# Performance work log

Measured on AMD Instinct MI355X. Metric: run time of the kernel, lower is better.

Reference implementation:

```python
import jax, jax.numpy as jnp
import numpy as np

A = 0.5  # mixing coefficient `a` from __init__
B, S, C = 16, 4096, 512


def setup_inputs() -> dict:
    key = jax.random.key(0)
    k1, k2 = jax.random.split(key)
    predicted = jax.random.normal(k1, (B, S, C), dtype=jnp.float32)
    target = jax.random.randint(k2, (B, S), 0, C, dtype=jnp.int64)
    return {"predicted": predicted, "target": target}


def reference(predicted, target):
    # predicted: [B, S, C] logits, target: [B, S] int class ids.
    b, s, c = predicted.shape
    am = jnp.argmax(predicted, axis=-1)              # [B, S] per-position top-1 class (topk(1)[1])
    lse = jax.nn.logsumexp(predicted, axis=-1)       # [B, S]

    # counts[i, j, v] = #positions s with target[i,s]==j and argmax==v
    bidx = jnp.arange(b)[:, None]
    counts = jnp.zeros((b, c, c), dtype=jnp.int32).at[bidx, target, am].add(1)
    n = counts.sum(axis=-1)                          # [B, C] occurrences of class j in target[i]
    # torch.mode returns the smallest of the most common values; argmax over class value
    # returns the first (smallest) index achieving the max count, matching that tie-break.
    m = jnp.argmax(counts, axis=-1)                  # [B, C] mode label per (i, j)

    # pred_m[i, j, s] = predicted[i, s, m[i, j]]
    pred_m = predicted[jnp.arange(b)[:, None, None],
                       jnp.arange(s)[None, None, :],
                       m[:, :, None]]                # [B, C, S]
    # per-position CE against constant label m: lse - logit[m]
    term = lse[:, None, :] - pred_m                  # [B, C, S]

    maskT = target[:, None, :] == jnp.arange(c)[None, :, None]  # [B, C, S]
    eq_sum = jnp.sum(jnp.where(maskT, term, 0.0), axis=-1)      # [B, C]
    ne_sum = term.sum(axis=-1) - eq_sum                          # [B, C]

    nf = n.astype(predicted.dtype)
    present = n > 0
    eq_loss = eq_sum / jnp.maximum(nf, 1.0)
    ne_mean = ne_sum / jnp.maximum(s - nf, 1.0)
    ne_loss = 1.0 / jnp.where(present & (ne_mean != 0), ne_mean, 1.0)
    val = eq_loss * (1.0 - A) + A * ne_loss          # [B, C]

    keep = present & (val != 0)                      # cipherLoss[cipherLoss != 0]
    total = jnp.where(keep, val, 0.0).sum()
    cnt = jnp.maximum(keep.sum(), 1).astype(predicted.dtype)
    return total / cnt
```

## Files before the change

kernel.cpp:

```cpp
#include <hip/hip_runtime.h>
#include <cstdint>
#include <cstddef>

#define PB 16
#define PS 4096
#define PC 512

__global__ __launch_bounds__(256) void k1_rows(const float* __restrict__ pred,
                                               int* __restrict__ am,
                                               float* __restrict__ lse,
                                               float* __restrict__ colsum) {
    const int t = threadIdx.x, w = t >> 6, l = t & 63;
    const int rowBase = blockIdx.x * 16 + w * 4;
    const int b = rowBase >> 12;
    const float* base = pred + (size_t)rowBase * PC + 4 * l;

    float4 va[4], vb[4];
    #pragma unroll
    for (int r = 0; r < 4; ++r) {
        va[r] = *(const float4*)(base + r * PC);
        vb[r] = *(const float4*)(base + r * PC + 256);
    }

    float mv[4]; int mi[4];
    #pragma unroll
    for (int r = 0; r < 4; ++r) {
        float m = va[r].x; int i0 = 4 * l;
        if (va[r].y > m) { m = va[r].y; i0 = 4 * l + 1; }
        if (va[r].z > m) { m = va[r].z; i0 = 4 * l + 2; }
        if (va[r].w > m) { m = va[r].w; i0 = 4 * l + 3; }
        if (vb[r].x > m) { m = vb[r].x; i0 = 256 + 4 * l; }
        if (vb[r].y > m) { m = vb[r].y; i0 = 256 + 4 * l + 1; }
        if (vb[r].z > m) { m = vb[r].z; i0 = 256 + 4 * l + 2; }
        if (vb[r].w > m) { m = vb[r].w; i0 = 256 + 4 * l + 3; }
        mv[r] = m; mi[r] = i0;
    }

    #pragma unroll
    for (int off = 1; off < 64; off <<= 1) {
        #pragma unroll
        for (int r = 0; r < 4; ++r) {
            float ov = __shfl_xor(mv[r], off, 64);
            int   oi = __shfl_xor(mi[r], off, 64);
            if (ov > mv[r] || (ov == mv[r] && oi < mi[r])) { mv[r] = ov; mi[r] = oi; }
        }
    }

    float ss[4];
    #pragma unroll
    for (int r = 0; r < 4; ++r) {
        ss[r] = __expf(va[r].x - mv[r]) + __expf(va[r].y - mv[r])
              + __expf(va[r].z - mv[r]) + __expf(va[r].w - mv[r])
              + __expf(vb[r].x - mv[r]) + __expf(vb[r].y - mv[r])
              + __expf(vb[r].z - mv[r]) + __expf(vb[r].w - mv[r]);
    }
    #pragma unroll
    for (int off = 1; off < 64; off <<= 1) {
        #pragma unroll
        for (int r = 0; r < 4; ++r) ss[r] += __shfl_xor(ss[r], off, 64);
    }

    float l0 = mv[0] + __logf(ss[0]);
    float l1 = mv[1] + __logf(ss[1]);
    float l2 = mv[2] + __logf(ss[2]);
    float l3 = mv[3] + __logf(ss[3]);

    if (l == 0) {
        *(float4*)(lse + rowBase) = make_float4(l0, l1, l2, l3);
        *(int4*)(am + rowBase) = make_int4(mi[0], mi[1], mi[2], mi[3]);
    }

    float cs0 = va[0].x + va[1].x + va[2].x + va[3].x;
    float cs1 = va[0].y + va[1].y + va[2].y + va[3].y;
    float cs2 = va[0].z + va[1].z + va[2].z + va[3].z;
    float cs3 = va[0].w + va[1].w + va[2].w + va[3].w;
    float cs4 = vb[0].x + vb[1].x + vb[2].x + vb[3].x;
    float cs5 = vb[0].y + vb[1].y + vb[2].y + vb[3].y;
    float cs6 = vb[0].z + vb[1].z + vb[2].z + vb[3].z;
    float cs7 = vb[0].w + vb[1].w + vb[2].w + vb[3].w;

    __shared__ float lds[4][PC];
    lds[w][4 * l + 0] = cs0; lds[w][4 * l + 1] = cs1;
    lds[w][4 * l + 2] = cs2; lds[w][4 * l + 3] = cs3;
    lds[w][256 + 4 * l + 0] = cs4; lds[w][256 + 4 * l + 1] = cs5;
    lds[w][256 + 4 * l + 2] = cs6; lds[w][256 + 4 * l + 3] = cs7;
    __syncthreads();
    for (int c = t; c < PC; c += 256) {
        float s = lds[0][c] + lds[1][c] + lds[2][c] + lds[3][c];
        atomicAdd(&colsum[(b << 9) + c], s);
    }
}

__global__ __launch_bounds__(1024) void k_tail(const float* __restrict__ pred,
                                               const int* __restrict__ target,
                                               const int* __restrict__ am,
                                               const float* __restrict__ lse,
                                               const float* __restrict__ colsum,
                                               float* __restrict__ acc,
                                               int* __restrict__ done,
                                               float* __restrict__ out) {
    __shared__ float ldsLse[PS];
    __shared__ int   sbucket[PS];
    __shared__ int   cnt[PC];
    __shared__ int   offsA[PC];
    __shared__ int   cur[PC];
    __shared__ float redL[16];
    __shared__ int   redS[8];
    __shared__ float redv[16], redk[16];

    const int b = blockIdx.x, t = threadIdx.x, w = t >> 6, l = t & 63;
    if (t < PC) cnt[t] = 0;
    __syncthreads();

    const int4*   tg4p = (const int4*)(target + (b << 12));
    const int4*   am4p = (const int4*)(am + (b << 12));
    const float4* ls4p = (const float4*)(lse + (b << 12));
    int4 tg4 = tg4p[t];
    int4 am4 = am4p[t];
    float4 ls4 = ls4p[t];
    ((float4*)ldsLse)[t] = ls4;
    atomicAdd(&cnt[tg4.x], 1);
    atomicAdd(&cnt[tg4.y], 1);
    atomicAdd(&cnt[tg4.z], 1);
    atomicAdd(&cnt[tg4.w], 1);
    float lacc = ls4.x + ls4.y + ls4.z + ls4.w;
    #pragma unroll
    for (int off = 1; off < 64; off <<= 1) lacc += __shfl_xor(lacc, off, 64);
    if (l == 0) redL[w] = lacc;
    __syncthreads();
    float Ls = 0.0f;
    #pragma unroll
    for (int j = 0; j < 16; ++j) Ls += redL[j];

    int x = 0, incl = 0;
    if (t < PC) {
        x = cnt[t];
        incl = x;
        #pragma unroll
        for (int off = 1; off < 64; off <<= 1) {
            int v = __shfl_up(incl, off, 64);
            if (l >= off) incl += v;
        }
        if (l == 63) redS[w] = incl;
    }
    __syncthreads();
    if (t < PC) {
        int woff = 0;
        #pragma unroll
        for (int j = 0; j < 8; ++j) woff += (j < w) ? redS[j] : 0;
        int excl = incl + woff - x;
        offsA[t] = excl;
        cur[t] = excl;
    }
    __syncthreads();

    {
        int pos;
        pos = atomicAdd(&cur[tg4.x], 1); sbucket[pos] = (4 * t + 0) | (am4.x << 12);
        pos = atomicAdd(&cur[tg4.y], 1); sbucket[pos] = (4 * t + 1) | (am4.y << 12);
        pos = atomicAdd(&cur[tg4.z], 1); sbucket[pos] = (4 * t + 2) | (am4.z << 12);
        pos = atomicAdd(&cur[tg4.w], 1); sbucket[pos] = (4 * t + 3) | (am4.w << 12);
    }
    __syncthreads();

    float val = 0.0f; int keep = 0;
    if (t < PC && x > 0) {
        int k = x, start = offsA[t];
        int bc = 0, bvv = 0;
        for (int i = 0; i < k; ++i) {
            int v = sbucket[start + i] >> 12;
            int c = 0;
            for (int j = 0; j < k; ++j) c += ((sbucket[start + j] >> 12) == v) ? 1 : 0;
            if (c > bc || (c == bc && v < bvv)) { bc = c; bvv = v; }
        }
        int m = bvv;
        float lseSum = 0.0f, ep0 = 0.0f, ep1 = 0.0f;
        const float* pb = pred + (size_t)(b << 12) * PC + m;
        int i = 0;
        for (; i + 1 < k; i += 2) {
            int s0 = sbucket[start + i] & (PS - 1);
            int s1 = sbucket[start + i + 1] & (PS - 1);
            lseSum += ldsLse[s0] + ldsLse[s1];
            ep0 += pb[(size_t)s0 * PC];
            ep1 += pb[(size_t)s1 * PC];
        }
        if (i < k) {
            int s0 = sbucket[start + i] & (PS - 1);
            lseSum += ldsLse[s0];
            ep0 += pb[(size_t)s0 * PC];
        }
        float eq_sum = lseSum - (ep0 + ep1);
        float ne_sum = (Ls - colsum[(b << 9) + m]) - eq_sum;
        float nf = (float)k;
        float eq_loss = eq_sum / fmaxf(nf, 1.0f);
        float ne_mean = ne_sum / fmaxf((float)PS - nf, 1.0f);
        float ne_loss = 1.0f / ((ne_mean != 0.0f) ? ne_mean : 1.0f);
        val = 0.5f * eq_loss + 0.5f * ne_loss;
        keep = (val != 0.0f) ? 1 : 0;
    }

    float vs = keep ? val : 0.0f;
    float ks = (float)keep;
    #pragma unroll
    for (int off = 1; off < 64; off <<= 1) {
        vs += __shfl_xor(vs, off, 64);
        ks += __shfl_xor(ks, off, 64);
    }
    if (l == 0) { redv[w] = vs; redk[w] = ks; }
    __syncthreads();
    if (t == 0) {
        float sv = 0.0f, sk = 0.0f;
        #pragma unroll
        for (int j = 0; j < 16; ++j) { sv += redv[j]; sk += redk[j]; }
        atomicAdd(&acc[0], sv);
        atomicAdd(&acc[1], sk);
        __threadfence();
        int d = atomicAdd(done, 1);
        if (d == PB - 1) {
            __threadfence();
            float a0 = atomicAdd(&acc[0], 0.0f);
            float a1 = atomicAdd(&acc[1], 0.0f);
            out[0] = a0 / fmaxf(a1, 1.0f);
        }
    }
}

extern "C" void kernel_launch(void* const* d_in, const int* in_sizes, int n_in,
                              void* d_out, int out_size, void* d_ws, size_t ws_size,
                              hipStream_t stream) {
    const float* pred = (const float*)d_in[0];
    const int* target = (const int*)d_in[1];
    float* out = (float*)d_out;

    char* w = (char*)d_ws;
    int*   am     = (int*)(w + 0);
    float* lse    = (float*)(w + 262144);
    float* colsum = (float*)(w + 524288);
    float* acc    = (float*)(w + 557056);
    int*   done   = (int*)(w + 557064);

    (void)hipMemsetAsync(w + 524288, 0, 32768 + 12, stream);
    k1_rows<<<(PB * PS) / 16, 256, 0, stream>>>(pred, am, lse, colsum);
    k_tail<<<PB, 1024, 0, stream>>>(pred, target, am, lse, colsum, acc, done, out);
}
```

Before: 218.9 us.

## Replace colsum atomics with per-block partials reduced in tail kernel

New measurement: 226.9 us. 3.7% more time.

```diff
diff --git a/kernel.cpp b/kernel.cpp
--- a/kernel.cpp
+++ b/kernel.cpp
@@ -9,85 +9,92 @@
 __global__ __launch_bounds__(256) void k1_rows(const float* __restrict__ pred,
                                                int* __restrict__ am,
                                                float* __restrict__ lse,
-                                               float* __restrict__ colsum) {
+                                               float* __restrict__ partial) {
     const int t = threadIdx.x, w = t >> 6, l = t & 63;
-    const int rowBase = blockIdx.x * 16 + w * 4;
-    const int b = rowBase >> 12;
-    const float* base = pred + (size_t)rowBase * PC + 4 * l;
-
-    float4 va[4], vb[4];
-    #pragma unroll
-    for (int r = 0; r < 4; ++r) {
-        va[r] = *(const float4*)(base + r * PC);
-        vb[r] = *(const float4*)(base + r * PC + 256);
-    }
-
-    float mv[4]; int mi[4];
-    #pragma unroll
-    for (int r = 0; r < 4; ++r) {
-        float m = va[r].x; int i0 = 4 * l;
-        if (va[r].y > m) { m = va[r].y; i0 = 4 * l + 1; }
-        if (va[r].z > m) { m = va[r].z; i0 = 4 * l + 2; }
-        if (va[r].w > m) { m = va[r].w; i0 = 4 * l + 3; }
-        if (vb[r].x > m) { m = vb[r].x; i0 = 256 + 4 * l; }
-        if (vb[r].y > m) { m = vb[r].y; i0 = 256 + 4 * l + 1; }
-        if (vb[r].z > m) { m = vb[r].z; i0 = 256 + 4 * l + 2; }
-        if (vb[r].w > m) { m = vb[r].w; i0 = 256 + 4 * l + 3; }
-        mv[r] = m; mi[r] = i0;
-    }
-
-    #pragma unroll
-    for (int off = 1; off < 64; off <<= 1) {
+    const int blockRow = blockIdx.x * 64;
+    const int b = blockRow >> 12;
+    const int waveRow = blockRow + w * 16;
+
+    float cs[8] = {0.f, 0.f, 0.f, 0.f, 0.f, 0.f, 0.f, 0.f};
+
+    #pragma unroll 2
+    for (int ch = 0; ch < 4; ++ch) {
+        const int rowBase = waveRow + ch * 4;
+        const float* base = pred + (size_t)rowBase * PC + 4 * l;
+
+        float4 va[4], vb[4];
         #pragma unroll
         for (int r = 0; r < 4; ++r) {
-            float ov = __shfl_xor(mv[r], off, 64);
-            int   oi = __shfl_xor(mi[r], off, 64);
-            if (ov > mv[r] || (ov == mv[r] && oi < mi[r])) { mv[r] = ov; mi[r] = oi; }
-        }
-    }
-
-    float ss[4];
-    #pragma unroll
-    for (int r = 0; r < 4; ++r) {
-        ss[r] = __expf(va[r].x - mv[r]) + __expf(va[r].y - mv[r])
-              + __expf(va[r].z - mv[r]) + __expf(va[r].w - mv[r])
-              + __expf(vb[r].x - mv[r]) + __expf(vb[r].y - mv[r])
-              + __expf(vb[r].z - mv[r]) + __expf(vb[r].w - mv[r]);
-    }
-    #pragma unroll
-    for (int off = 1; off < 64; off <<= 1) {
-        #pragma unroll
-        for (int r = 0; r < 4; ++r) ss[r] += __shfl_xor(ss[r], off, 64);
-    }
-
-    float l0 = mv[0] + __logf(ss[0]);
-    float l1 = mv[1] + __logf(ss[1]);
-    float l2 = mv[2] + __logf(ss[2]);
-    float l3 = mv[3] + __logf(ss[3]);
-
-    if (l == 0) {
-        *(float4*)(lse + rowBase) = make_float4(l0, l1, l2, l3);
-        *(int4*)(am + rowBase) = make_int4(mi[0], mi[1], mi[2], mi[3]);
-    }
-
-    float cs0 = va[0].x + va[1].x + va[2].x + va[3].x;
-    float cs1 = va[0].y + va[1].y + va[2].y + va[3].y;
-    float cs2 = va[0].z + va[1].z + va[2].z + va[3].z;
-    float cs3 = va[0].w + va[1].w + va[2].w + va[3].w;
-    float cs4 = vb[0].x + vb[1].x + vb[2].x + vb[3].x;
-    float cs5 = vb[0].y + vb[1].y + vb[2].y + vb[3].y;
-    float cs6 = vb[0].z + vb[1].z + vb[2].z + vb[3].z;
-    float cs7 = vb[0].w + vb[1].w + vb[2].w + vb[3].w;
+            va[r] = *(const float4*)(base + r * PC);
+            vb[r] = *(const float4*)(base + r * PC + 256);
+        }
+
+        float mv[4]; int mi[4];
+        #pragma unroll
+        for (int r = 0; r < 4; ++r) {
+            float m = va[r].x; int i0 = 4 * l;
+            if (va[r].y > m) { m = va[r].y; i0 = 4 * l + 1; }
+            if (va[r].z > m) { m = va[r].z; i0 = 4 * l + 2; }
+            if (va[r].w > m) { m = va[r].w; i0 = 4 * l + 3; }
+            if (vb[r].x > m) { m = vb[r].x; i0 = 256 + 4 * l; }
+            if (vb[r].y > m) { m = vb[r].y; i0 = 256 + 4 * l + 1; }
+            if (vb[r].z > m) { m = vb[r].z; i0 = 256 + 4 * l + 2; }
+            if (vb[r].w > m) { m = vb[r].w; i0 = 256 + 4 * l + 3; }
+            mv[r] = m; mi[r] = i0;
+        }
+
+        #pragma unroll
+        for (int off = 1; off < 64; off <<= 1) {
+            #pragma unroll
+            for (int r = 0; r < 4; ++r) {
+                float ov = __shfl_xor(mv[r], off, 64);
+                int   oi = __shfl_xor(mi[r], off, 64);
+                if (ov > mv[r] || (ov == mv[r] && oi < mi[r])) { mv[r] = ov; mi[r] = oi; }
+            }
+        }
+
+        float ss[4];
+        #pragma unroll
+        for (int r = 0; r < 4; ++r) {
+            ss[r] = __expf(va[r].x - mv[r]) + __expf(va[r].y - mv[r])
+                  + __expf(va[r].z - mv[r]) + __expf(va[r].w - mv[r])
+                  + __expf(vb[r].x - mv[r]) + __expf(vb[r].y - mv[r])
+                  + __expf(vb[r].z - mv[r]) + __expf(vb[r].w - mv[r]);
+        }
+        #pragma unroll
+        for (int off = 1; off < 64; off <<= 1) {
+            #pragma unroll
+            for (int r = 0; r < 4; ++r) ss[r] += __shfl_xor(ss[r], off, 64);
+        }
+
+        if (l == 0) {
+            float l0 = mv[0] + __logf(ss[0]);
+            float l1 = mv[1] + __logf(ss[1]);
+            float l2 = mv[2] + __logf(ss[2]);
+            float l3 = mv[3] + __logf(ss[3]);
+            *(float4*)(lse + rowBase) = make_float4(l0, l1, l2, l3);
+            *(int4*)(am + rowBase) = make_int4(mi[0], mi[1], mi[2], mi[3]);
+        }
+
+        cs[0] += va[0].x + va[1].x + va[2].x + va[3].x;
+        cs[1] += va[0].y + va[1].y + va[2].y + va[3].y;
+        cs[2] += va[0].z + va[1].z + va[2].z + va[3].z;
+        cs[3] += va[0].w + va[1].w + va[2].w + va[3].w;
+        cs[4] += vb[0].x + vb[1].x + vb[2].x + vb[3].x;
+        cs[5] += vb[0].y + vb[1].y + vb[2].y + vb[3].y;
+        cs[6] += vb[0].z + vb[1].z + vb[2].z + vb[3].z;
+        cs[7] += vb[0].w + vb[1].w + vb[2].w + vb[3].w;
+    }
 
     __shared__ float lds[4][PC];
-    lds[w][4 * l + 0] = cs0; lds[w][4 * l + 1] = cs1;
-    lds[w][4 * l + 2] = cs2; lds[w][4 * l + 3] = cs3;
-    lds[w][256 + 4 * l + 0] = cs4; lds[w][256 + 4 * l + 1] = cs5;
-    lds[w][256 + 4 * l + 2] = cs6; lds[w][256 + 4 * l + 3] = cs7;
-    __syncthreads();
+    lds[w][4 * l + 0] = cs[0]; lds[w][4 * l + 1] = cs[1];
+    lds[w][4 * l + 2] = cs[2]; lds[w][4 * l + 3] = cs[3];
+    lds[w][256 + 4 * l + 0] = cs[4]; lds[w][256 + 4 * l + 1] = cs[5];
+    lds[w][256 + 4 * l + 2] = cs[6]; lds[w][256 + 4 * l + 3] = cs[7];
+    __syncthreads();
+    float* pout = partial + (size_t)blockIdx.x * PC;
     for (int c = t; c < PC; c += 256) {
-        float s = lds[0][c] + lds[1][c] + lds[2][c] + lds[3][c];
-        atomicAdd(&colsum[(b << 9) + c], s);
+        pout[c] = lds[0][c] + lds[1][c] + lds[2][c] + lds[3][c];
     }
 }
 
@@ -95,7 +102,7 @@
                                                const int* __restrict__ target,
                                                const int* __restrict__ am,
                                                const float* __restrict__ lse,
-                                               const float* __restrict__ colsum,
+                                               const float* __restrict__ partial,
                                                float* __restrict__ acc,
                                                int* __restrict__ done,
                                                float* __restrict__ out) {
@@ -104,6 +111,7 @@
     __shared__ int   cnt[PC];
     __shared__ int   offsA[PC];
     __shared__ int   cur[PC];
+    __shared__ float colS[PC];
     __shared__ float redL[16];
     __shared__ int   redS[8];
     __shared__ float redv[16], redk[16];
@@ -111,6 +119,14 @@
     const int b = blockIdx.x, t = threadIdx.x, w = t >> 6, l = t & 63;
     if (t < PC) cnt[t] = 0;
     __syncthreads();
+
+    if (t < PC) {
+        const float* pp = partial + (size_t)(b * 64) * PC + t;
+        float s = 0.0f;
+        #pragma unroll 8
+        for (int g = 0; g < 64; ++g) s += pp[(size_t)g * PC];
+        colS[t] = s;
+    }
 
     const int4*   tg4p = (const int4*)(target + (b << 12));
     const int4*   am4p = (const int4*)(am + (b << 12));
@@ -190,7 +206,7 @@
             ep0 += pb[(size_t)s0 * PC];
         }
         float eq_sum = lseSum - (ep0 + ep1);
-        float ne_sum = (Ls - colsum[(b << 9) + m]) - eq_sum;
+        float ne_sum = (Ls - colS[m]) - eq_sum;
         float nf = (float)k;
         float eq_loss = eq_sum / fmaxf(nf, 1.0f);
         float ne_mean = ne_sum / fmaxf((float)PS - nf, 1.0f);
@@ -233,13 +249,13 @@
     float* out = (float*)d_out;
 
     char* w = (char*)d_ws;
-    int*   am     = (int*)(w + 0);
-    float* lse    = (float*)(w + 262144);
-    float* colsum = (float*)(w + 524288);
-    float* acc    = (float*)(w + 557056);
-    int*   done   = (int*)(w + 557064);
-
-    (void)hipMemsetAsync(w + 524288, 0, 32768 + 12, stream);
-    k1_rows<<<(PB * PS) / 16, 256, 0, stream>>>(pred, am, lse, colsum);
-    k_tail<<<PB, 1024, 0, stream>>>(pred, target, am, lse, colsum, acc, done, out);
+    int*   am      = (int*)(w + 0);
+    float* lse     = (float*)(w + 262144);
+    float* partial = (float*)(w + 524288);
+    float* acc     = (float*)(w + 2621440);
+    int*   done    = (int*)(w + 2621448);
+
+    (void)hipMemsetAsync(w + 2621440, 0, 12, stream);
+    k1_rows<<<(PB * PS) / 64, 256, 0, stream>>>(pred, am, lse, partial);
+    k_tail<<<PB, 1024, 0, stream>>>(pred, target, am, lse, partial, acc, done, out);
 }
```
